# Performance work log

Measured on AMD Instinct MI355X. Metric: run time of the kernel, lower is better.

## Reference

```python
import jax, jax.numpy as jnp
from jax import lax
import numpy as np

INPUT_SIZE, HIDDEN, NUM_LAYERS, OUTPUT = 64, 512, 2, 1024
BATCH, SEQ = 64, 1024


def setup_inputs() -> dict:
    key = jax.random.key(0)
    ks = jax.random.split(key, 11)
    s = 1.0 / np.sqrt(HIDDEN)
    u = lambda k, shape: jax.random.uniform(k, shape, jnp.float32, -s, s)
    return {
        "x": jax.random.normal(ks[0], (BATCH, SEQ, INPUT_SIZE), jnp.float32),
        # layer 0 (PyTorch gate order: i, f, g, o stacked along dim 0)
        "W_ih0": u(ks[1], (4 * HIDDEN, INPUT_SIZE)),
        "W_hh0": u(ks[2], (4 * HIDDEN, HIDDEN)),
        "b_ih0": u(ks[3], (4 * HIDDEN,)),
        "b_hh0": u(ks[4], (4 * HIDDEN,)),
        # layer 1
        "W_ih1": u(ks[5], (4 * HIDDEN, HIDDEN)),
        "W_hh1": u(ks[6], (4 * HIDDEN, HIDDEN)),
        "b_ih1": u(ks[7], (4 * HIDDEN,)),
        "b_hh1": u(ks[8], (4 * HIDDEN,)),
        # fc
        "fc_w": u(ks[9], (OUTPUT, HIDDEN)),
        "fc_b": u(ks[10], (OUTPUT,)),
    }


def _lstm_layer(x, W_ih, W_hh, b_ih, b_hh):
    # x: [B, T, D]. Precompute input projection for all timesteps (one big GEMM).
    B = x.shape[0]
    H = W_hh.shape[1]
    xw = jnp.einsum('btd,gd->btg', x, W_ih) + b_ih + b_hh  # [B, T, 4H]
    xw = jnp.swapaxes(xw, 0, 1)  # [T, B, 4H] for scan
    h0 = jnp.zeros((B, H), x.dtype)
    c0 = jnp.zeros((B, H), x.dtype)

    def step(carry, xw_t):
        h, c = carry
        gates = xw_t + h @ W_hh.T  # [B, 4H]
        i, f, g, o = jnp.split(gates, 4, axis=-1)
        c = jax.nn.sigmoid(f) * c + jax.nn.sigmoid(i) * jnp.tanh(g)
        h = jax.nn.sigmoid(o) * jnp.tanh(c)
        return (h, c), h

    (h_T, c_T), hs = lax.scan(step, (h0, c0), xw)
    return jnp.swapaxes(hs, 0, 1), h_T  # [B, T, H], [B, H]


def _forward(x, W_ih0, W_hh0, b_ih0, b_hh0, W_ih1, W_hh1, b_ih1, b_hh1, fc_w, fc_b):
    ula0, h0_T = _lstm_layer(x, W_ih0, W_hh0, b_ih0, b_hh0)
    ula1, h1_T = _lstm_layer(ula0, W_ih1, W_hh1, b_ih1, b_hh1)
    # h_out: [num_layers, B, H] -> view(-1, H)
    h_out = jnp.concatenate([h0_T, h1_T], axis=0)  # [L*B, H]
    out = h_out @ fc_w.T + fc_b
    out = jax.nn.relu(out)
    # Dropout(p=0.2): identity in eval mode (deterministic reference)
    return out


def reference(x, W_ih0, W_hh0, b_ih0, b_hh0, W_ih1, W_hh1, b_ih1, b_hh1, fc_w, fc_b):
    return _forward(x, W_ih0, W_hh0, b_ih0, b_hh0, W_ih1, W_hh1, b_ih1, b_hh1, fc_w, fc_b)
```

## Files before the change

kernel.cpp:

```cpp
#include <hip/hip_runtime.h>


#define H      512
#define T_SEQ  1024
#define DIN    64
#define STEPS  1025

#define GRP_STRIDE_U32  49152
#define SLOT_STRIDE_U32 16384
#define WS_BYTES        (4 * GRP_STRIDE_U32 * 4)

typedef _Float16 f16x8 __attribute__((ext_vector_type(8)));
typedef float    f32x4 __attribute__((ext_vector_type(4)));

__device__ __forceinline__ unsigned long long ld_u64(const unsigned long long* p) {
  return __hip_atomic_load((unsigned long long*)p, __ATOMIC_RELAXED, __HIP_MEMORY_SCOPE_AGENT);
}
__device__ __forceinline__ void st_u32(unsigned* p, unsigned v) {
  __hip_atomic_store(p, v, __ATOMIC_RELAXED, __HIP_MEMORY_SCOPE_AGENT);
}
__device__ __forceinline__ f16x8 pk8(float4 a, float4 b) {
  f16x8 r;
  r[0] = (_Float16)a.x; r[1] = (_Float16)a.y; r[2] = (_Float16)a.z; r[3] = (_Float16)a.w;
  r[4] = (_Float16)b.x; r[5] = (_Float16)b.y; r[6] = (_Float16)b.z; r[7] = (_Float16)b.w;
  return r;
}
__device__ __forceinline__ f16x8 cvt8(const float* p) {
  return pk8(*(const float4*)p, *(const float4*)(p + 4));
}
__device__ __forceinline__ f32x4 mfma16(f16x8 a, f16x8 b, f32x4 c) {
  return __builtin_amdgcn_mfma_f32_16x16x32_f16(a, b, c, 0, 0, 0);
}
__device__ __forceinline__ float rcpf_(float x) {
#if __has_builtin(__builtin_amdgcn_rcpf)
  return __builtin_amdgcn_rcpf(x);
#else
  return 1.0f / x;
#endif
}
__device__ __forceinline__ float sigm(float x) {
  x = fminf(fmaxf(x, -30.f), 30.f);
  return rcpf_(1.f + __expf(-x));
}
__device__ __forceinline__ float tanhx(float x) {
  x = fminf(fmaxf(x, -15.f), 15.f);
  float e = __expf(2.f * x);
  return (e - 1.f) * rcpf_(e + 1.f);
}

__global__ __launch_bounds__(256, 1)
void lstm_fused(const float* __restrict__ x,
                const float* __restrict__ Wih0, const float* __restrict__ Whh0,
                const float* __restrict__ bih0, const float* __restrict__ bhh0,
                const float* __restrict__ Wih1, const float* __restrict__ Whh1,
                const float* __restrict__ bih1, const float* __restrict__ bhh1,
                const float* __restrict__ fcw,  const float* __restrict__ fcb,
                float* __restrict__ out, unsigned* __restrict__ ws)
{
  __shared__ unsigned sH[2 * 16 * 260];

  const int tid   = threadIdx.x;
  const int wid   = blockIdx.x;
  const int g     = wid >> 6;
  const int w     = wid & 63;
  const int wave  = tid >> 6;
  const int lane  = tid & 63;
  const int layer = wave >> 1;
  const int hb    = w * 8 + (wave & 1) * 4;
  const int bcol  = lane & 15;
  const int kgrp  = lane >> 4;

  unsigned* gbase = ws + g * GRP_STRIDE_U32;

  const int src_m = lane & 15;
  const int grow  = (src_m & 3) * H + hb + (src_m >> 2);
  f16x8 wA[32];
  if (layer == 0) {
    #pragma unroll
    for (int ks = 0; ks < 18; ++ks) {
      int kk = ks * 32 + kgrp * 8;
      const float* p = (kk < DIN) ? (Wih0 + (size_t)grow * DIN + kk)
                                  : (Whh0 + (size_t)grow * H + (kk - DIN));
      wA[ks] = cvt8(p);
    }
  } else {
    #pragma unroll
    for (int ks = 0; ks < 32; ++ks) {
      int kk = ks * 32 + kgrp * 8;
      const float* p = (kk < H) ? (Wih1 + (size_t)grow * H + kk)
                                : (Whh1 + (size_t)grow * H + (kk - H));
      wA[ks] = cvt8(p);
    }
  }
  const int hown = hb + kgrp;
  float bias[4];
  {
    const float* bi = layer ? bih1 : bih0;
    const float* bh = layer ? bhh1 : bhh0;
    #pragma unroll
    for (int r = 0; r < 4; ++r) { int rr = r * H + hown; bias[r] = bi[rr] + bh[rr]; }
  }

  for (int i = tid; i < 2 * 16 * 260; i += 256) sH[i] = 0;
  __syncthreads();

  float c = 0.f;
  unsigned spins = 0;
  const int rowb = bcol * 1040 + kgrp * 16;

  for (int s = 0; s < STEPS; ++s) {
    float4 xr0 = {0,0,0,0}, xr1 = xr0, xr2 = xr0, xr3 = xr0;
    if (layer == 0) {
      int t = (s < T_SEQ) ? s : (T_SEQ - 1);
      const float* xp = x + ((size_t)((g * 16 + bcol) * T_SEQ + t)) * DIN + kgrp * 8;
      xr0 = *(const float4*)xp;        xr1 = *(const float4*)(xp + 4);
      xr2 = *(const float4*)(xp + 32); xr3 = *(const float4*)(xp + 36);
    }
    if (s > 0) {
      const unsigned long long* src =
          (const unsigned long long*)(gbase + ((s - 1) % 3) * SLOT_STRIDE_U32);
      const unsigned want = (unsigned)s;
      unsigned long long v[32];
      #pragma unroll
      for (int i = 0; i < 32; ++i) v[i] = ld_u64(src + tid + i * 256);
      for (;;) {
        unsigned bad = 0;
        #pragma unroll
        for (int i = 0; i < 32; ++i) {
          unsigned lo = (unsigned)v[i], hi = (unsigned)(v[i] >> 32);
          if (((lo >> 16) ^ want) | ((hi >> 16) ^ want)) bad |= (1u << i);
        }
        if (!bad) break;
        if (++spins > 2000000u) break;
        #pragma unroll
        for (int i = 0; i < 32; ++i)
          if (bad & (1u << i)) v[i] = ld_u64(src + tid + i * 256);
      }
      #pragma unroll
      for (int i = 0; i < 32; ++i) {
        int j = tid + i * 256;
        unsigned payload = ((unsigned)v[i] & 0xffffu) | ((unsigned)(v[i] >> 32) << 16);
        sH[(j >> 12) * 4160 + ((j >> 8) & 15) * 260 + (j & 255)] = payload;
      }
    }
    __syncthreads();

    const bool active = layer ? (s > 0) : (s < T_SEQ);
    float hval = 0.f;
    if (active) {
      f32x4 acc[4] = {{0,0,0,0},{0,0,0,0},{0,0,0,0},{0,0,0,0}};
      const char* b0 = (const char*)sH;
      const char* b1 = (const char*)sH + 16640;
      if (layer == 0) {
        acc[0] = mfma16(wA[0], pk8(xr0, xr1), acc[0]);
        acc[1] = mfma16(wA[1], pk8(xr2, xr3), acc[1]);
        #pragma unroll
        for (int ks = 2; ks < 18; ++ks) {
          f16x8 bf = *(const f16x8*)(b0 + rowb + ks * 64 - 128);
          acc[ks & 3] = mfma16(wA[ks], bf, acc[ks & 3]);
        }
      } else {
        #pragma unroll
        for (int ks = 0; ks < 16; ++ks) {
          f16x8 bf = *(const f16x8*)(b0 + rowb + ks * 64);
          acc[ks & 3] = mfma16(wA[ks], bf, acc[ks & 3]);
        }
        #pragma unroll
        for (int ks = 16; ks < 32; ++ks) {
          f16x8 bf = *(const f16x8*)(b1 + rowb + (ks - 16) * 64);
          acc[ks & 3] = mfma16(wA[ks], bf, acc[ks & 3]);
        }
      }
      f32x4 a = (acc[0] + acc[1]) + (acc[2] + acc[3]);
      float ii = sigm(a[0] + bias[0]);
      float ff = sigm(a[1] + bias[1]);
      float gt = tanhx(a[2] + bias[2]);
      float oo = sigm(a[3] + bias[3]);
      c = ff * c + ii * gt;
      hval = oo * tanhx(c);
    }
    const bool produce = layer ? true : (s < T_SEQ);
    if (produce) {
      _Float16 hf = (_Float16)hval;
      unsigned hu = (unsigned)__builtin_bit_cast(unsigned short, hf);
      unsigned word = hu | ((unsigned)(s + 1) << 16);
      unsigned* dst = gbase + (s % 3) * SLOT_STRIDE_U32 + layer * 8192
                    + bcol * 512 + hown;
      st_u32(dst, word);
    }
    __syncthreads();
  }

  if (wid < 128) {
    const int rt = wid >> 4, ct = wid & 15;
    const int sg = rt & 3;
    const bool isH1 = (rt >= 4);
    const unsigned want = isH1 ? (unsigned)(STEPS + 0) : (unsigned)(STEPS - 1);
    const int     slot  = isH1 ? 1 : 0;
    const unsigned long long* src =
        (const unsigned long long*)(ws + sg * GRP_STRIDE_U32
                                    + slot * SLOT_STRIDE_U32 + (isH1 ? 8192 : 0));
    unsigned long long v[16];
    #pragma unroll
    for (int i = 0; i < 16; ++i) v[i] = ld_u64(src + tid + i * 256);
    for (;;) {
      unsigned bad = 0;
      #pragma unroll
      for (int i = 0; i < 16; ++i) {
        unsigned lo = (unsigned)v[i], hi = (unsigned)(v[i] >> 32);
        if (((lo >> 16) ^ want) | ((hi >> 16) ^ want)) bad |= (1u << i);
      }
      if (!bad) break;
      if (++spins > 2000000u) break;
      #pragma unroll
      for (int i = 0; i < 16; ++i)
        if (bad & (1u << i)) v[i] = ld_u64(src + tid + i * 256);
    }
    #pragma unroll
    for (int i = 0; i < 16; ++i) {
      int j = tid + i * 256;
      unsigned payload = ((unsigned)v[i] & 0xffffu) | ((unsigned)(v[i] >> 32) << 16);
      sH[(j >> 8) * 260 + (j & 255)] = payload;
    }
    __syncthreads();
    const int col = ct * 64 + wave * 16 + bcol;
    f32x4 a0 = {0,0,0,0}, a1 = {0,0,0,0};
    #pragma unroll
    for (int ks = 0; ks < 16; ++ks) {
      f16x8 af = *(const f16x8*)((const char*)sH + rowb + ks * 64);
      f16x8 bf = cvt8(fcw + (size_t)col * H + ks * 32 + kgrp * 8);
      if (ks & 1) a1 = mfma16(af, bf, a1); else a0 = mfma16(af, bf, a0);
    }
    f32x4 a = a0 + a1;
    const float fb = fcb[col];
    #pragma unroll
    for (int r = 0; r < 4; ++r) {
      int row = rt * 16 + kgrp * 4 + r;
      float v2 = a[r] + fb;
      out[(size_t)row * 1024 + col] = v2 > 0.f ? v2 : 0.f;
    }
  }
}

extern "C" void kernel_launch(void* const* d_in, const int* in_sizes, int n_in,
                              void* d_out, int out_size, void* d_ws, size_t ws_size,
                              hipStream_t stream) {
  const float* x    = (const float*)d_in[0];
  const float* Wih0 = (const float*)d_in[1];
  const float* Whh0 = (const float*)d_in[2];
  const float* bih0 = (const float*)d_in[3];
  const float* bhh0 = (const float*)d_in[4];
  const float* Wih1 = (const float*)d_in[5];
  const float* Whh1 = (const float*)d_in[6];
  const float* bih1 = (const float*)d_in[7];
  const float* bhh1 = (const float*)d_in[8];
  const float* fcw  = (const float*)d_in[9];
  const float* fcb  = (const float*)d_in[10];
  (void)in_sizes; (void)n_in; (void)out_size; (void)ws_size;

  hipMemsetAsync(d_ws, 0, WS_BYTES, stream);
  lstm_fused<<<dim3(256), dim3(256), 0, stream>>>(
      x, Wih0, Whh0, bih0, bhh0, Wih1, Whh1, bih1, bhh1, fcw, fcb,
      (float*)d_out, (unsigned*)d_ws);
}
```

Baseline: 4.995 ms.

## Halve block count, split K across helper waves with LDS partial-sum reduction

The persistent kernel moves from 256 blocks of 4 waves to 128 blocks of 8 waves. Each wave now owns 8 hidden units (two MFMA tiles), and the K dimension is split between "final" and "helper" waves, which combine their partial sums through an LDS buffer before the gate nonlinearity. The aim is to cut the number of blocks that poll the global handoff buffer each step and to balance per-wave MFMA work; s_sleep is also added to the spin loop. The cost is an extra __syncthreads and an LDS round-trip on every step of the recurrence.

```diff
diff --git a/kernel.cpp b/kernel.cpp
--- a/kernel.cpp
+++ b/kernel.cpp
@@ -6,9 +6,9 @@
 #define DIN    64
 #define STEPS  1025
 
-#define GRP_STRIDE_U32  49152
-#define SLOT_STRIDE_U32 16384
-#define WS_BYTES        (4 * GRP_STRIDE_U32 * 4)
+#define SLOT_U32 16384
+#define GRP_U32  49152
+#define WS_BYTES (4 * GRP_U32 * 4)
 
 typedef _Float16 f16x8 __attribute__((ext_vector_type(8)));
 typedef float    f32x4 __attribute__((ext_vector_type(4)));
@@ -48,7 +48,7 @@
   return (e - 1.f) * rcpf_(e + 1.f);
 }
 
-__global__ __launch_bounds__(256, 1)
+__global__ __launch_bounds__(512, 2)
 void lstm_fused(const float* __restrict__ x,
                 const float* __restrict__ Wih0, const float* __restrict__ Whh0,
                 const float* __restrict__ bih0, const float* __restrict__ bhh0,
@@ -57,60 +57,89 @@
                 const float* __restrict__ fcw,  const float* __restrict__ fcb,
                 float* __restrict__ out, unsigned* __restrict__ ws)
 {
-  __shared__ unsigned sH[2 * 16 * 260];
-
-  const int tid   = threadIdx.x;
-  const int wid   = blockIdx.x;
-  const int g     = wid >> 6;
-  const int w     = wid & 63;
-  const int wave  = tid >> 6;
-  const int lane  = tid & 63;
-  const int layer = wave >> 1;
-  const int hb    = w * 8 + (wave & 1) * 4;
-  const int bcol  = lane & 15;
-  const int kgrp  = lane >> 4;
-
-  unsigned* gbase = ws + g * GRP_STRIDE_U32;
+  __shared__ unsigned sH[2 * 16 * 260 + 2048];
+  float* pb = (float*)(sH + 8320);
+
+  const int tid  = threadIdx.x;
+  const int wid  = blockIdx.x;
+  const int g    = wid >> 5;
+  const int w    = wid & 31;
+  const int wv   = tid >> 6;
+  const int lane = tid & 63;
+  const int bcol = lane & 15;
+  const int kgrp = lane >> 4;
+  const int U0   = w * 16;
+
+  const int layer    = (wv >= 2 && wv <= 5) ? 1 : 0;
+  const int hb       = U0 + ((wv == 1 || wv == 7 || wv == 4 || wv == 5) ? 8 : 0);
+  const bool is_final  = (wv == 0 || wv == 1 || wv == 2 || wv == 4);
+  const bool is_helper = !is_final;
+
+  unsigned* gbase = ws + g * GRP_U32;
 
   const int src_m = lane & 15;
-  const int grow  = (src_m & 3) * H + hb + (src_m >> 2);
-  f16x8 wA[32];
-  if (layer == 0) {
-    #pragma unroll
-    for (int ks = 0; ks < 18; ++ks) {
-      int kk = ks * 32 + kgrp * 8;
-      const float* p = (kk < DIN) ? (Wih0 + (size_t)grow * DIN + kk)
-                                  : (Whh0 + (size_t)grow * H + (kk - DIN));
-      wA[ks] = cvt8(p);
+  const int gr0 = (src_m & 3) * H + hb + (src_m >> 2);
+  const int gr1 = gr0 + 4;
+  f16x8 wA[2][16];
+  if (wv <= 1) {
+    #pragma unroll
+    for (int f = 0; f < 9; ++f) {
+      const float *p0, *p1;
+      if (f < 2) {
+        p0 = Wih0 + (size_t)gr0 * DIN + f * 32 + kgrp * 8;
+        p1 = Wih0 + (size_t)gr1 * DIN + f * 32 + kgrp * 8;
+      } else {
+        p0 = Whh0 + (size_t)gr0 * H + (f - 2) * 32 + kgrp * 8;
+        p1 = Whh0 + (size_t)gr1 * H + (f - 2) * 32 + kgrp * 8;
+      }
+      wA[0][f] = cvt8(p0); wA[1][f] = cvt8(p1);
+    }
+  } else if (wv >= 6) {
+    #pragma unroll
+    for (int q = 0; q < 9; ++q) {
+      int col = (q + 7) * 32 + kgrp * 8;
+      wA[0][q] = cvt8(Whh0 + (size_t)gr0 * H + col);
+      wA[1][q] = cvt8(Whh0 + (size_t)gr1 * H + col);
+    }
+  } else if (wv == 2 || wv == 4) {
+    #pragma unroll
+    for (int f = 0; f < 16; ++f) {
+      int col = f * 32 + kgrp * 8;
+      wA[0][f] = cvt8(Wih1 + (size_t)gr0 * H + col);
+      wA[1][f] = cvt8(Wih1 + (size_t)gr1 * H + col);
     }
   } else {
     #pragma unroll
-    for (int ks = 0; ks < 32; ++ks) {
-      int kk = ks * 32 + kgrp * 8;
-      const float* p = (kk < H) ? (Wih1 + (size_t)grow * H + kk)
-                                : (Whh1 + (size_t)grow * H + (kk - H));
-      wA[ks] = cvt8(p);
+    for (int q = 0; q < 16; ++q) {
+      int col = q * 32 + kgrp * 8;
+      wA[0][q] = cvt8(Whh1 + (size_t)gr0 * H + col);
+      wA[1][q] = cvt8(Whh1 + (size_t)gr1 * H + col);
     }
   }
-  const int hown = hb + kgrp;
-  float bias[4];
-  {
+
+  float bias[2][4];
+  if (is_final) {
     const float* bi = layer ? bih1 : bih0;
     const float* bh = layer ? bhh1 : bhh0;
     #pragma unroll
-    for (int r = 0; r < 4; ++r) { int rr = r * H + hown; bias[r] = bi[rr] + bh[rr]; }
+    for (int t = 0; t < 2; ++t)
+      #pragma unroll
+      for (int r = 0; r < 4; ++r) {
+        int u = hb + t * 4 + kgrp;
+        bias[t][r] = bi[r * H + u] + bh[r * H + u];
+      }
   }
 
-  for (int i = tid; i < 2 * 16 * 260; i += 256) sH[i] = 0;
+  for (int i = tid; i < 2 * 16 * 260; i += 512) sH[i] = 0;
   __syncthreads();
 
-  float c = 0.f;
+  float cst0 = 0.f, cst1 = 0.f;
   unsigned spins = 0;
   const int rowb = bcol * 1040 + kgrp * 16;
 
   for (int s = 0; s < STEPS; ++s) {
     float4 xr0 = {0,0,0,0}, xr1 = xr0, xr2 = xr0, xr3 = xr0;
-    if (layer == 0) {
+    if (wv <= 1) {
       int t = (s < T_SEQ) ? s : (T_SEQ - 1);
       const float* xp = x + ((size_t)((g * 16 + bcol) * T_SEQ + t)) * DIN + kgrp * 8;
       xr0 = *(const float4*)xp;        xr1 = *(const float4*)(xp + 4);
@@ -118,126 +147,162 @@
     }
     if (s > 0) {
       const unsigned long long* src =
-          (const unsigned long long*)(gbase + ((s - 1) % 3) * SLOT_STRIDE_U32);
+          (const unsigned long long*)(gbase + ((s - 1) % 3) * SLOT_U32);
       const unsigned want = (unsigned)s;
-      unsigned long long v[32];
-      #pragma unroll
-      for (int i = 0; i < 32; ++i) v[i] = ld_u64(src + tid + i * 256);
+      unsigned long long v[16];
+      #pragma unroll
+      for (int i = 0; i < 16; ++i) v[i] = ld_u64(src + tid + i * 512);
       for (;;) {
         unsigned bad = 0;
         #pragma unroll
-        for (int i = 0; i < 32; ++i) {
+        for (int i = 0; i < 16; ++i) {
           unsigned lo = (unsigned)v[i], hi = (unsigned)(v[i] >> 32);
           if (((lo >> 16) ^ want) | ((hi >> 16) ^ want)) bad |= (1u << i);
         }
         if (!bad) break;
         if (++spins > 2000000u) break;
-        #pragma unroll
-        for (int i = 0; i < 32; ++i)
-          if (bad & (1u << i)) v[i] = ld_u64(src + tid + i * 256);
-      }
-      #pragma unroll
-      for (int i = 0; i < 32; ++i) {
-        int j = tid + i * 256;
+        __builtin_amdgcn_s_sleep(1);
+        #pragma unroll
+        for (int i = 0; i < 16; ++i)
+          if (bad & (1u << i)) v[i] = ld_u64(src + tid + i * 512);
+      }
+      #pragma unroll
+      for (int i = 0; i < 16; ++i) {
+        int j = tid + i * 512;
         unsigned payload = ((unsigned)v[i] & 0xffffu) | ((unsigned)(v[i] >> 32) << 16);
         sH[(j >> 12) * 4160 + ((j >> 8) & 15) * 260 + (j & 255)] = payload;
       }
     }
     __syncthreads();
 
-    const bool active = layer ? (s > 0) : (s < T_SEQ);
-    float hval = 0.f;
-    if (active) {
-      f32x4 acc[4] = {{0,0,0,0},{0,0,0,0},{0,0,0,0},{0,0,0,0}};
-      const char* b0 = (const char*)sH;
-      const char* b1 = (const char*)sH + 16640;
-      if (layer == 0) {
-        acc[0] = mfma16(wA[0], pk8(xr0, xr1), acc[0]);
-        acc[1] = mfma16(wA[1], pk8(xr2, xr3), acc[1]);
-        #pragma unroll
-        for (int ks = 2; ks < 18; ++ks) {
-          f16x8 bf = *(const f16x8*)(b0 + rowb + ks * 64 - 128);
-          acc[ks & 3] = mfma16(wA[ks], bf, acc[ks & 3]);
+    const bool act = layer ? (s > 0) : (s < T_SEQ);
+    f32x4 acc0 = {0,0,0,0}, acc1 = {0,0,0,0};
+    if (act) {
+      const char* base0 = (const char*)sH;
+      const char* base1 = (const char*)sH + 16640;
+      if (wv <= 1) {
+        f16x8 b0 = pk8(xr0, xr1);
+        acc0 = mfma16(wA[0][0], b0, acc0); acc1 = mfma16(wA[1][0], b0, acc1);
+        f16x8 b1 = pk8(xr2, xr3);
+        acc0 = mfma16(wA[0][1], b1, acc0); acc1 = mfma16(wA[1][1], b1, acc1);
+        #pragma unroll
+        for (int f = 2; f < 9; ++f) {
+          f16x8 bf = *(const f16x8*)(base0 + rowb + (f - 2) * 64);
+          acc0 = mfma16(wA[0][f], bf, acc0); acc1 = mfma16(wA[1][f], bf, acc1);
+        }
+      } else if (wv >= 6) {
+        #pragma unroll
+        for (int q = 0; q < 9; ++q) {
+          f16x8 bf = *(const f16x8*)(base0 + rowb + (q + 7) * 64);
+          acc0 = mfma16(wA[0][q], bf, acc0); acc1 = mfma16(wA[1][q], bf, acc1);
+        }
+      } else if (wv == 2 || wv == 4) {
+        #pragma unroll
+        for (int f = 0; f < 16; ++f) {
+          f16x8 bf = *(const f16x8*)(base0 + rowb + f * 64);
+          acc0 = mfma16(wA[0][f], bf, acc0); acc1 = mfma16(wA[1][f], bf, acc1);
         }
       } else {
         #pragma unroll
-        for (int ks = 0; ks < 16; ++ks) {
-          f16x8 bf = *(const f16x8*)(b0 + rowb + ks * 64);
-          acc[ks & 3] = mfma16(wA[ks], bf, acc[ks & 3]);
-        }
-        #pragma unroll
-        for (int ks = 16; ks < 32; ++ks) {
-          f16x8 bf = *(const f16x8*)(b1 + rowb + (ks - 16) * 64);
-          acc[ks & 3] = mfma16(wA[ks], bf, acc[ks & 3]);
-        }
-      }
-      f32x4 a = (acc[0] + acc[1]) + (acc[2] + acc[3]);
-      float ii = sigm(a[0] + bias[0]);
-      float ff = sigm(a[1] + bias[1]);
-      float gt = tanhx(a[2] + bias[2]);
-      float oo = sigm(a[3] + bias[3]);
-      c = ff * c + ii * gt;
-      hval = oo * tanhx(c);
-    }
-    const bool produce = layer ? true : (s < T_SEQ);
-    if (produce) {
-      _Float16 hf = (_Float16)hval;
-      unsigned hu = (unsigned)__builtin_bit_cast(unsigned short, hf);
-      unsigned word = hu | ((unsigned)(s + 1) << 16);
-      unsigned* dst = gbase + (s % 3) * SLOT_STRIDE_U32 + layer * 8192
-                    + bcol * 512 + hown;
-      st_u32(dst, word);
+        for (int q = 0; q < 16; ++q) {
+          f16x8 bf = *(const f16x8*)(base1 + rowb + q * 64);
+          acc0 = mfma16(wA[0][q], bf, acc0); acc1 = mfma16(wA[1][q], bf, acc1);
+        }
+      }
+    }
+    if (is_helper && act) {
+      const int pidx = (wv == 6) ? 0 : (wv == 7) ? 1 : (wv == 3) ? 2 : 3;
+      *(f32x4*)&pb[(pidx * 2 + 0) * 256 + lane * 4] = acc0;
+      *(f32x4*)&pb[(pidx * 2 + 1) * 256 + lane * 4] = acc1;
     }
     __syncthreads();
+    if (is_final) {
+      float hv0 = 0.f, hv1 = 0.f;
+      if (act) {
+        const int pidx = (wv == 0) ? 0 : (wv == 1) ? 1 : (wv == 2) ? 2 : 3;
+        acc0 += *(const f32x4*)&pb[(pidx * 2 + 0) * 256 + lane * 4];
+        acc1 += *(const f32x4*)&pb[(pidx * 2 + 1) * 256 + lane * 4];
+        {
+          float ii = sigm(acc0[0] + bias[0][0]);
+          float ff = sigm(acc0[1] + bias[0][1]);
+          float gg = tanhx(acc0[2] + bias[0][2]);
+          float oo = sigm(acc0[3] + bias[0][3]);
+          cst0 = ff * cst0 + ii * gg;
+          hv0 = oo * tanhx(cst0);
+        }
+        {
+          float ii = sigm(acc1[0] + bias[1][0]);
+          float ff = sigm(acc1[1] + bias[1][1]);
+          float gg = tanhx(acc1[2] + bias[1][2]);
+          float oo = sigm(acc1[3] + bias[1][3]);
+          cst1 = ff * cst1 + ii * gg;
+          hv1 = oo * tanhx(cst1);
+        }
+      }
+      const bool produce = layer ? true : (s < T_SEQ);
+      if (produce) {
+        unsigned tag = (unsigned)(s + 1) << 16;
+        unsigned u0 = (unsigned)__builtin_bit_cast(unsigned short, (_Float16)hv0);
+        unsigned u1 = (unsigned)__builtin_bit_cast(unsigned short, (_Float16)hv1);
+        unsigned* dst = gbase + (s % 3) * SLOT_U32 + layer * 8192
+                      + bcol * 512 + hb + kgrp;
+        st_u32(dst,     u0 | tag);
+        st_u32(dst + 4, u1 | tag);
+      }
+    }
   }
 
-  if (wid < 128) {
+  __syncthreads();
+  {
     const int rt = wid >> 4, ct = wid & 15;
     const int sg = rt & 3;
     const bool isH1 = (rt >= 4);
-    const unsigned want = isH1 ? (unsigned)(STEPS + 0) : (unsigned)(STEPS - 1);
+    const unsigned want = isH1 ? (unsigned)STEPS : (unsigned)(STEPS - 1);
     const int     slot  = isH1 ? 1 : 0;
     const unsigned long long* src =
-        (const unsigned long long*)(ws + sg * GRP_STRIDE_U32
-                                    + slot * SLOT_STRIDE_U32 + (isH1 ? 8192 : 0));
-    unsigned long long v[16];
-    #pragma unroll
-    for (int i = 0; i < 16; ++i) v[i] = ld_u64(src + tid + i * 256);
+        (const unsigned long long*)(ws + sg * GRP_U32 + slot * SLOT_U32
+                                    + (isH1 ? 8192 : 0));
+    unsigned long long v[8];
+    #pragma unroll
+    for (int i = 0; i < 8; ++i) v[i] = ld_u64(src + tid + i * 512);
     for (;;) {
       unsigned bad = 0;
       #pragma unroll
-      for (int i = 0; i < 16; ++i) {
+      for (int i = 0; i < 8; ++i) {
         unsigned lo = (unsigned)v[i], hi = (unsigned)(v[i] >> 32);
         if (((lo >> 16) ^ want) | ((hi >> 16) ^ want)) bad |= (1u << i);
       }
       if (!bad) break;
       if (++spins > 2000000u) break;
-      #pragma unroll
-      for (int i = 0; i < 16; ++i)
-        if (bad & (1u << i)) v[i] = ld_u64(src + tid + i * 256);
-    }
-    #pragma unroll
-    for (int i = 0; i < 16; ++i) {
-      int j = tid + i * 256;
+      __builtin_amdgcn_s_sleep(1);
+      #pragma unroll
+      for (int i = 0; i < 8; ++i)
+        if (bad & (1u << i)) v[i] = ld_u64(src + tid + i * 512);
+    }
+    #pragma unroll
+    for (int i = 0; i < 8; ++i) {
+      int j = tid + i * 512;
       unsigned payload = ((unsigned)v[i] & 0xffffu) | ((unsigned)(v[i] >> 32) << 16);
       sH[(j >> 8) * 260 + (j & 255)] = payload;
     }
     __syncthreads();
-    const int col = ct * 64 + wave * 16 + bcol;
-    f32x4 a0 = {0,0,0,0}, a1 = {0,0,0,0};
-    #pragma unroll
-    for (int ks = 0; ks < 16; ++ks) {
-      f16x8 af = *(const f16x8*)((const char*)sH + rowb + ks * 64);
-      f16x8 bf = cvt8(fcw + (size_t)col * H + ks * 32 + kgrp * 8);
-      if (ks & 1) a1 = mfma16(af, bf, a1); else a0 = mfma16(af, bf, a0);
-    }
-    f32x4 a = a0 + a1;
-    const float fb = fcb[col];
-    #pragma unroll
-    for (int r = 0; r < 4; ++r) {
-      int row = rt * 16 + kgrp * 4 + r;
-      float v2 = a[r] + fb;
-      out[(size_t)row * 1024 + col] = v2 > 0.f ? v2 : 0.f;
+    if (wv < 4) {
+      const int col = ct * 64 + wv * 16 + bcol;
+      f32x4 a0 = {0,0,0,0}, a1 = {0,0,0,0};
+      #pragma unroll
+      for (int f = 0; f < 16; ++f) {
+        f16x8 af = *(const f16x8*)((const char*)sH + rowb + f * 64);
+        f16x8 bf = cvt8(fcw + (size_t)col * H + f * 32 + kgrp * 8);
+        if (f & 1) a1 = mfma16(af, bf, a1); else a0 = mfma16(af, bf, a0);
+      }
+      f32x4 a = a0 + a1;
+      const float fb = fcb[col];
+      #pragma unroll
+      for (int r = 0; r < 4; ++r) {
+        int row = rt * 16 + kgrp * 4 + r;
+        float v2 = a[r] + fb;
+        out[(size_t)row * 1024 + col] = v2 > 0.f ? v2 : 0.f;
+      }
     }
   }
 }
@@ -259,7 +324,7 @@
   (void)in_sizes; (void)n_in; (void)out_size; (void)ws_size;
 
   hipMemsetAsync(d_ws, 0, WS_BYTES, stream);
-  lstm_fused<<<dim3(256), dim3(256), 0, stream>>>(
+  lstm_fused<<<dim3(128), dim3(512), 0, stream>>>(
       x, Wih0, Whh0, bih0, bhh0, Wih1, Whh1, bih1, bhh1, fcw, fcb,
       (float*)d_out, (unsigned*)d_ws);
 }
```

Measured after the change: 7.124 ms. +42.6%, slower.
